# Kernel tuning notes

Measured on AMD Instinct MI355X. Metric: run time of the kernel, lower is better.

## Reference

```python
import jax, jax.numpy as jnp
import numpy as np
from jax import lax

H, W = 3072, 4096
BLACK = 0.0625            # black level (normalized)
KNEE_X = np.array([0.0, 0.25, 1.0], np.float32)   # decompanding curve
KNEE_Y = np.array([0.0, 0.50, 1.0], np.float32)
DEN_R, DEN_EPS = 2, 100.0         # BayerDenoise defaults
AWB_MAX_GAIN = 4.0
LTM_A, LTM_B, LTM_R, LTM_EPS = 0.7, 0.0, 8, 1e-3
GAMMA = 2.2


def _box_sum_1d(x, r, axis):
    """Sliding-window sum of width 2r+1 along `axis`, edge-truncated."""
    n = x.shape[axis]
    c = jnp.cumsum(x, axis=axis)
    hi = jnp.clip(jnp.arange(n) + r, 0, n - 1)
    lo = jnp.arange(n) - r - 1
    upper = jnp.take(c, hi, axis=axis)
    lower = jnp.take(c, jnp.clip(lo, 0, n - 1), axis=axis)
    shp = [1] * x.ndim
    shp[axis] = n
    lower = lower * (lo >= 0).astype(x.dtype).reshape(shp)
    return upper - lower


def box_mean(x, r):
    """2D box mean over last two axes, normalized by valid window counts."""
    s = _box_sum_1d(_box_sum_1d(x, r, -2), r, -1)
    cnt = _box_sum_1d(_box_sum_1d(jnp.ones_like(x), r, -2), r, -1)
    return s / cnt


def guided_self(I, r, eps):
    """Self-guided (edge-preserving) filter."""
    m = box_mean(I, r)
    var = box_mean(I * I, r) - m * m
    a = var / (var + eps)
    b = m * (1.0 - a)
    return box_mean(a, r) * I + box_mean(b, r)


def conv3x3(img, k):
    return lax.conv_general_dilated(img[None, None], k[None, None], (1, 1), 'SAME')[0, 0]


def isp_pipeline(x, ccm):
    # --- DecompandBlackLevel: piecewise-linear decompand + black level ---
    x = jnp.interp(x, jnp.asarray(KNEE_X), jnp.asarray(KNEE_Y))
    x = jnp.clip((x - BLACK) / (1.0 - BLACK), 0.0, 1.0)

    # --- BayerDenoise: guided filter on each RGGB plane ---
    p = jnp.stack([x[0::2, 0::2], x[0::2, 1::2], x[1::2, 0::2], x[1::2, 1::2]])  # [4,H/2,W/2]
    p = guided_self(p, DEN_R, DEN_EPS)

    # --- AWB: gray-world gains from plane means (lum mask [0,1] = all pixels) ---
    r_m, g_m, b_m = p[0].mean(), 0.5 * (p[1].mean() + p[2].mean()), p[3].mean()
    gr = jnp.minimum(g_m / (r_m + 1e-8), AWB_MAX_GAIN)
    gb = jnp.minimum(g_m / (b_m + 1e-8), AWB_MAX_GAIN)
    x = (jnp.zeros_like(x)
         .at[0::2, 0::2].set(jnp.clip(p[0] * gr, 0.0, 1.0))
         .at[0::2, 1::2].set(jnp.clip(p[1], 0.0, 1.0))
         .at[1::2, 0::2].set(jnp.clip(p[2], 0.0, 1.0))
         .at[1::2, 1::2].set(jnp.clip(p[3] * gb, 0.0, 1.0)))

    # --- Demosaic: bilinear on RGGB mosaic ---
    ii = (jnp.arange(H) % 2)[:, None]
    jj = (jnp.arange(W) % 2)[None, :]
    mR = ((ii == 0) & (jj == 0)).astype(x.dtype)
    mG = (ii != jj).astype(x.dtype)
    mB = ((ii == 1) & (jj == 1)).astype(x.dtype)
    k_g = jnp.array([[0, 1, 0], [1, 4, 1], [0, 1, 0]], jnp.float32) / 4.0
    k_rb = jnp.array([[1, 2, 1], [2, 4, 2], [1, 2, 1]], jnp.float32) / 4.0
    rgb = jnp.stack([conv3x3(x * mR, k_rb), conv3x3(x * mG, k_g), conv3x3(x * mB, k_rb)])  # [3,H,W]

    # --- CCM ---
    rgb = jnp.clip(jnp.einsum('ij,jhw->ihw', ccm, rgb), 0.0, 1.0)

    wl = jnp.array([0.299, 0.587, 0.114], jnp.float32)
    Y = jnp.einsum('c,chw->hw', wl, rgb)
    Ys = Y.reshape(H // 2, 2, W // 2, 2).mean(axis=(1, 3))
    base = jax.image.resize(guided_self(Ys, LTM_R, LTM_EPS), (H, W), 'bilinear')
    Ynew = LTM_A * base + LTM_B + (Y - base)       # detail_gain=1, threshold=0
    rgb = jnp.clip(rgb * (Ynew / (Y + 1e-6)), 0.0, 1.0)

    # --- Gamma ---
    rgb = jnp.clip(rgb, 1e-6, 1.0) ** (1.0 / GAMMA)
    # hist_norm / post_denoise / saturation / sharpening are identity at defaults

    # --- RGBtoYUV -> NV12 (full range BT.601) ---
    R, G, B = rgb[0], rgb[1], rgb[2]
    Yf = 0.299 * R + 0.587 * G + 0.114 * B
    U = -0.168736 * R - 0.331264 * G + 0.5 * B + 0.5
    V = 0.5 * R - 0.418688 * G - 0.081312 * B + 0.5
    Us = U.reshape(H // 2, 2, W // 2, 2).mean(axis=(1, 3))
    Vs = V.reshape(H // 2, 2, W // 2, 2).mean(axis=(1, 3))
    uv = jnp.stack([Us, Vs], axis=-1).reshape(H // 2, W)  # interleaved UVUV...
    out = jnp.concatenate([Yf.reshape(-1), uv.reshape(-1)]) * 255.0
    return jnp.clip(out, 0.0, 255.0)   # float NV12 codes (pre-quantization)


def setup_inputs() -> dict:
    key = jax.random.key(0)
    k1, k2 = jax.random.split(key)
    x = jax.random.uniform(k1, (H, W), dtype=jnp.float32)
    ccm = jnp.eye(3, dtype=jnp.float32) + 0.1 * jax.random.normal(k2, (3, 3), dtype=jnp.float32)
    return {"x": x, "ccm": ccm}


def reference(x, ccm):
    return isp_pipeline(x, ccm)
```

## Files before the change

kernel.cpp:

```cpp
#include <hip/hip_runtime.h>
#include <math.h>

#define IMG_H 3072
#define IMG_W 4096
#define Hh 1536
#define Wh 2048
#define S (Hh*Wh)

#define TID 32
#define TIL 16

#if __has_builtin(__builtin_amdgcn_rcpf)
#define RCP(x) __builtin_amdgcn_rcpf(x)
#else
#define RCP(x) (1.0f/(x))
#endif

__device__ __forceinline__ float clamp01(float v){ return fminf(fmaxf(v, 0.0f), 1.0f); }

__device__ __forceinline__ float decompand_black(float v){
  float y = (v <= 0.25f) ? (2.0f*v) : fmaf(v - 0.25f, 0.5f/0.75f, 0.5f);
  y = clamp01(y);
  return clamp01((y - 0.0625f) * (1.0f/0.9375f));
}

__device__ __forceinline__ float gamma22(float x){
  return __builtin_amdgcn_exp2f(0.45454545454545453f * __builtin_amdgcn_logf(x));
}

__global__ __launch_bounds__(256) void k_split(const float* __restrict__ x, float* __restrict__ P,
                                               float* __restrict__ sums){
  int idx = blockIdx.x*256 + threadIdx.x;
  int i = idx >> 10, jq = (idx & 1023)*2;
  const float* r0 = x + (size_t)(2*i)*IMG_W + 2*jq;
  float4 a = *(const float4*)r0;
  float4 b = *(const float4*)(r0 + IMG_W);
  size_t o = (size_t)i*Wh + jq;
  *(float2*)(P + o)            = make_float2(decompand_black(a.x), decompand_black(a.z));
  *(float2*)(P + S + o)        = make_float2(decompand_black(a.y), decompand_black(a.w));
  *(float2*)(P + 2*(size_t)S + o) = make_float2(decompand_black(b.x), decompand_black(b.z));
  *(float2*)(P + 3*(size_t)S + o) = make_float2(decompand_black(b.y), decompand_black(b.w));
  if (blockIdx.x == 0 && threadIdx.x < 4) sums[threadIdx.x] = 0.f;
}

template<int TI, bool FAST>
__device__ __forceinline__ void denoise_col2(const float* __restrict__ in, float* __restrict__ D,
                                             int c0, int i0, float& local){
  const float inv25 = 1.0f/25.0f;
  float cw_a[6], amask[6], cw_o0 = 25.f, cw_o1 = 25.f;
  if (!FAST){
    #pragma unroll
    for (int k=0;k<6;++k){
      int pc = c0 + k - 2;
      bool ok = ((unsigned)pc < (unsigned)Wh);
      amask[k] = ok ? 1.f : 0.f;
      cw_a[k]  = ok ? (float)(min(pc+2, Wh-1) - max(pc-2, 0) + 1) : 1.f;
    }
    cw_o0 = (float)(min(c0+2, Wh-1)   - max(c0-2, 0) + 1);
    cw_o1 = (float)(min(c0+3, Wh-1)   - max(c0-1, 0) + 1);
  }

  float rh1[6][5]={{0}}, rh2[6][5]={{0}};
  float vs1[6]={0}, vs2[6]={0};
  float rha0[5]={0}, rhb0[5]={0}, rha1[5]={0}, rhb1[5]={0};
  float cI0[5]={0}, cI1[5]={0};
  float wa0=0.f, wb0=0.f, wa1=0.f, wb1=0.f;

  const float* rp = in + (size_t)(i0-4)*Wh + c0;
  float* wp = D + (size_t)i0*Wh + c0;

  #pragma unroll 4
  for (int rr=0; rr<TI+8; ++rr){
    int r = i0 - 4 + rr;
    float v[10];
    if (FAST){
      float2 p0 = *(const float2*)(rp-4);
      float2 p1 = *(const float2*)(rp-2);
      float2 p2 = *(const float2*)(rp);
      float2 p3 = *(const float2*)(rp+2);
      float2 p4 = *(const float2*)(rp+4);
      v[0]=p0.x; v[1]=p0.y; v[2]=p1.x; v[3]=p1.y; v[4]=p2.x;
      v[5]=p2.y; v[6]=p3.x; v[7]=p3.y; v[8]=p4.x; v[9]=p4.y;
    } else {
      if ((unsigned)r < (unsigned)Hh){
        #pragma unroll
        for (int d=0; d<10; ++d){
          int c = c0 + d - 4;
          v[d] = ((unsigned)c < (unsigned)Wh) ? rp[d-4] : 0.f;
        }
      } else {
        #pragma unroll
        for (int d=0; d<10; ++d) v[d]=0.f;
      }
    }
    rp += Wh;
    float sq[10];
    #pragma unroll
    for (int d=0; d<10; ++d) sq[d]=v[d]*v[d];
    float h1[6], h2[6];
    h1[0]=v[0]+v[1]+v[2]+v[3]+v[4];
    h2[0]=sq[0]+sq[1]+sq[2]+sq[3]+sq[4];
    #pragma unroll
    for (int k=1;k<6;++k){
      h1[k]=h1[k-1]-v[k-1]+v[k+4];
      h2[k]=h2[k-1]-sq[k-1]+sq[k+4];
    }
    #pragma unroll
    for (int k=0;k<6;++k){
      vs1[k]+=h1[k]-rh1[k][0];
      vs2[k]+=h2[k]-rh2[k][0];
      #pragma unroll
      for (int t=0;t<4;++t){ rh1[k][t]=rh1[k][t+1]; rh2[k][t]=rh2[k][t+1]; }
      rh1[k][4]=h1[k]; rh2[k][4]=h2[k];
    }
    #pragma unroll
    for (int t=0;t<4;++t){ cI0[t]=cI0[t+1]; cI1[t]=cI1[t+1]; }
    cI0[4]=v[4]; cI1[4]=v[5];

    if (rr >= 4){
      int q = r-2;
      float a6[6], b6[6];
      if (FAST){
        #pragma unroll
        for (int k=0;k<6;++k){
          float m   = vs1[k]*inv25;
          float var = fmaf(-m, m, vs2[k]*inv25);
          float a   = var*RCP(var + 100.0f);
          a6[k] = a; b6[k] = fmaf(-m, a, m);
        }
      } else {
        float rmask = ((unsigned)q < (unsigned)Hh) ? 1.f : 0.f;
        float rh = (float)(min(q+2, Hh-1) - max(q-2, 0) + 1);
        #pragma unroll
        for (int k=0;k<6;++k){
          float inv = RCP(rh*cw_a[k]);
          float m   = vs1[k]*inv;
          float var = fmaf(-m, m, vs2[k]*inv);
          float a   = var*RCP(var + 100.0f);
          float b   = fmaf(-m, a, m);
          a6[k] = a*amask[k]*rmask; b6[k] = b*amask[k]*rmask;
        }
      }
      float ha0 = a6[0]+a6[1]+a6[2]+a6[3]+a6[4];
      float hb0 = b6[0]+b6[1]+b6[2]+b6[3]+b6[4];
      float ha1 = ha0 - a6[0] + a6[5];
      float hb1 = hb0 - b6[0] + b6[5];
      wa0 += ha0 - rha0[0]; wb0 += hb0 - rhb0[0];
      wa1 += ha1 - rha1[0]; wb1 += hb1 - rhb1[0];
      #pragma unroll
      for (int t=0;t<4;++t){
        rha0[t]=rha0[t+1]; rhb0[t]=rhb0[t+1];
        rha1[t]=rha1[t+1]; rhb1[t]=rhb1[t+1];
      }
      rha0[4]=ha0; rhb0[4]=hb0; rha1[4]=ha1; rhb1[4]=hb1;

      if (rr >= 8){
        int ro = r-4;
        float invo0, invo1;
        if (FAST){ invo0 = inv25; invo1 = inv25; }
        else {
          float rho = (float)(min(ro+2, Hh-1) - max(ro-2, 0) + 1);
          invo0 = RCP(rho*cw_o0); invo1 = RCP(rho*cw_o1);
        }
        float d0 = fmaf(wa0*invo0, cI0[0], wb0*invo0);
        float d1 = fmaf(wa1*invo1, cI1[0], wb1*invo1);
        *(float2*)wp = make_float2(d0, d1); wp += Wh;
        local += d0 + d1;
      }
    }
  }
}

template<int TI>
__global__ __launch_bounds__(256) void k_denoise(const float* __restrict__ P4,
                                                 float* __restrict__ D4,
                                                 float* __restrict__ sums){
  const int c0 = (blockIdx.x*256 + threadIdx.x)*2;
  const int i0 = blockIdx.y*TI;
  const int pl = blockIdx.z;
  const float* __restrict__ in = P4 + (size_t)pl*S;
  float* __restrict__ D = D4 + (size_t)pl*S;
  float local = 0.f;

  const int cmin = (blockIdx.x*256 + (threadIdx.x & ~63))*2;
  const bool rows_ok = (i0 >= 4) && (i0 + TI + 4 <= Hh);
  const bool fast = rows_ok && (cmin >= 4) && (cmin + 131 < Wh);
  if (fast) denoise_col2<TI, true >(in, D, c0, i0, local);
  else      denoise_col2<TI, false>(in, D, c0, i0, local);

  __shared__ float red[256];
  red[threadIdx.x]=local;
  __syncthreads();
  #pragma unroll
  for (int off=128; off>0; off>>=1){
    if (threadIdx.x<off) red[threadIdx.x]+=red[threadIdx.x+off];
    __syncthreads();
  }
  if (threadIdx.x==0) atomicAdd(sums+pl, red[0]);
}

template<int R, int TI>
__global__ __launch_bounds__(256) void k_boxsq_ab(const float* __restrict__ in,
                                                  float* __restrict__ A, float* __restrict__ B,
                                                  float eps){
  int j  = blockIdx.x*256 + threadIdx.x;
  int i0 = blockIdx.y*TI;
  int cw = min(j+R, Wh-1) - max(j-R, 0) + 1;

  float hs[2*R+1], hs2[2*R+1];
  float ws = 0.f, ws2 = 0.f;
  #pragma unroll
  for (int k=0; k<2*R+1; ++k){
    int r = i0 - R + k;
    float s = 0.f, s2 = 0.f;
    if ((unsigned)r < (unsigned)Hh){
      const float* row = in + r*Wh;
      #pragma unroll
      for (int d=-R; d<=R; ++d){
        int c = j + d;
        float v = ((unsigned)c < (unsigned)Wh) ? row[c] : 0.f;
        s += v; s2 = fmaf(v, v, s2);
      }
    }
    hs[k] = s; hs2[k] = s2; ws += s; ws2 += s2;
  }
  #pragma unroll
  for (int t=0; t<TI; ++t){
    int i = i0 + t;
    int rh = min(i+R, Hh-1) - max(i-R, 0) + 1;
    float inv = 1.0f/(float)(rh*cw);
    float m   = ws*inv;
    float var = fmaf(-m, m, ws2*inv);
    float a   = var/(var + eps);
    A[i*Wh + j] = a;
    B[i*Wh + j] = m*(1.0f - a);
    if (t < TI-1){
      ws -= hs[0]; ws2 -= hs2[0];
      #pragma unroll
      for (int k=0; k<2*R; ++k){ hs[k]=hs[k+1]; hs2[k]=hs2[k+1]; }
      int r = i + R + 1;
      float s = 0.f, s2 = 0.f;
      if (r < Hh){
        const float* row = in + r*Wh;
        #pragma unroll
        for (int d=-R; d<=R; ++d){
          int c = j + d;
          float v = ((unsigned)c < (unsigned)Wh) ? row[c] : 0.f;
          s += v; s2 = fmaf(v, v, s2);
        }
      }
      hs[2*R] = s; hs2[2*R] = s2; ws += s; ws2 += s2;
    }
  }
}

template<int R, int TI>
__global__ __launch_bounds__(256) void k_box_apply(const float* __restrict__ in,
                                                   const float* __restrict__ A, const float* __restrict__ B,
                                                   float* __restrict__ D){
  int j  = blockIdx.x*256 + threadIdx.x;
  int i0 = blockIdx.y*TI;
  int cw = min(j+R, Wh-1) - max(j-R, 0) + 1;

  float ha[2*R+1], hb[2*R+1];
  float wa = 0.f, wb = 0.f;
  #pragma unroll
  for (int k=0; k<2*R+1; ++k){
    int r = i0 - R + k;
    float sa = 0.f, sb = 0.f;
    if ((unsigned)r < (unsigned)Hh){
      const float* ra = A + r*Wh;
      const float* rb = B + r*Wh;
      #pragma unroll
      for (int d=-R; d<=R; ++d){
        int c = j + d;
        bool ok = ((unsigned)c < (unsigned)Wh);
        sa += ok ? ra[c] : 0.f;
        sb += ok ? rb[c] : 0.f;
      }
    }
    ha[k] = sa; hb[k] = sb; wa += sa; wb += sb;
  }
  #pragma unroll
  for (int t=0; t<TI; ++t){
    int i = i0 + t;
    int rh = min(i+R, Hh-1) - max(i-R, 0) + 1;
    float inv = 1.0f/(float)(rh*cw);
    D[i*Wh + j] = fmaf(wa*inv, in[i*Wh + j], wb*inv);
    if (t < TI-1){
      wa -= ha[0]; wb -= hb[0];
      #pragma unroll
      for (int k=0; k<2*R; ++k){ ha[k]=ha[k+1]; hb[k]=hb[k+1]; }
      int r = i + R + 1;
      float sa = 0.f, sb = 0.f;
      if (r < Hh){
        const float* ra = A + r*Wh;
        const float* rb = B + r*Wh;
        #pragma unroll
        for (int d2=-R; d2<=R; ++d2){
          int c = j + d2;
          bool ok = ((unsigned)c < (unsigned)Wh);
          sa += ok ? ra[c] : 0.f;
          sb += ok ? rb[c] : 0.f;
        }
      }
      ha[2*R] = sa; hb[2*R] = sb; wa += sa; wb += sb;
    }
  }
}

__device__ __forceinline__ void awb_gains(const float* __restrict__ sums, float& gr, float& gb){
  const float invS = 1.0f/(float)S;
  float rm = sums[0]*invS, g1 = sums[1]*invS, g2 = sums[2]*invS, bm = sums[3]*invS;
  float gm = 0.5f*(g1+g2);
  gr = fminf(gm/(rm + 1e-8f), 4.0f);
  gb = fminf(gm/(bm + 1e-8f), 4.0f);
}

__device__ __forceinline__ void load_mosaic2(const float* __restrict__ D, float gr, float gb,
                                             int i, int j, float m[4][6]){
  const float* __restrict__ P0 = D;
  const float* __restrict__ P1 = D + (size_t)S;
  const float* __restrict__ P2 = D + (size_t)2*S;
  const float* __restrict__ P3 = D + (size_t)3*S;
  const bool up = (i > 0), dn = (i < Hh-1), lf = (j > 0), rt = (j+2 < Wh);
  const size_t rc = (size_t)i*Wh + j;
  const size_t ru = rc - Wh, rd = rc + Wh;
  const float2 z = make_float2(0.f, 0.f);
  {
    float2 t3 = up ? *(const float2*)(P3+ru) : z;
    float2 t2 = up ? *(const float2*)(P2+ru) : z;
    m[0][0] = (up&&lf) ? clamp01(P3[ru-1]*gb) : 0.f;
    m[0][1] = clamp01(t2.x);
    m[0][2] = clamp01(t3.x*gb);
    m[0][3] = clamp01(t2.y);
    m[0][4] = clamp01(t3.y*gb);
    m[0][5] = (up&&rt) ? clamp01(P2[ru+2]) : 0.f;
  }
  {
    float2 t1 = *(const float2*)(P1+rc);
    float2 t0 = *(const float2*)(P0+rc);
    m[1][0] = lf ? clamp01(P1[rc-1]) : 0.f;
    m[1][1] = clamp01(t0.x*gr);
    m[1][2] = clamp01(t1.x);
    m[1][3] = clamp01(t0.y*gr);
    m[1][4] = clamp01(t1.y);
    m[1][5] = rt ? clamp01(P0[rc+2]*gr) : 0.f;
  }
  {
    float2 s3 = *(const float2*)(P3+rc);
    float2 s2 = *(const float2*)(P2+rc);
    m[2][0] = lf ? clamp01(P3[rc-1]*gb) : 0.f;
    m[2][1] = clamp01(s2.x);
    m[2][2] = clamp01(s3.x*gb);
    m[2][3] = clamp01(s2.y);
    m[2][4] = clamp01(s3.y*gb);
    m[2][5] = rt ? clamp01(P2[rc+2]) : 0.f;
  }
  {
    float2 u1 = dn ? *(const float2*)(P1+rd) : z;
    float2 u0 = dn ? *(const float2*)(P0+rd) : z;
    m[3][0] = (dn&&lf) ? clamp01(P1[rd-1]) : 0.f;
    m[3][1] = clamp01(u0.x*gr);
    m[3][2] = clamp01(u1.x);
    m[3][3] = clamp01(u0.y*gr);
    m[3][4] = clamp01(u1.y);
    m[3][5] = (dn&&rt) ? clamp01(P0[rd+2]*gr) : 0.f;
  }
}

template<int O>
__device__ __forceinline__ void demosaic_ccm_s(const float m[4][6], const float* __restrict__ C,
                                               float R[2][2], float G[2][2], float Bv[2][2]){
  #define MM(a,b) m[a][(b)+2*O]
  float r[2][2], g[2][2], b[2][2];
  r[0][0] = MM(1,1);
  g[0][0] = 0.25f*(MM(0,1)+MM(2,1)+MM(1,0)+MM(1,2));
  b[0][0] = 0.25f*(MM(0,0)+MM(0,2)+MM(2,0)+MM(2,2));
  r[0][1] = 0.5f*(MM(1,1)+MM(1,3));
  g[0][1] = MM(1,2);
  b[0][1] = 0.5f*(MM(0,2)+MM(2,2));
  r[1][0] = 0.5f*(MM(1,1)+MM(3,1));
  g[1][0] = MM(2,1);
  b[1][0] = 0.5f*(MM(2,0)+MM(2,2));
  r[1][1] = 0.25f*(MM(1,1)+MM(1,3)+MM(3,1)+MM(3,3));
  g[1][1] = 0.25f*(MM(1,2)+MM(3,2)+MM(2,1)+MM(2,3));
  b[1][1] = MM(2,2);
  #undef MM
  #pragma unroll
  for (int a=0; a<2; ++a){
    #pragma unroll
    for (int c=0; c<2; ++c){
      R[a][c]  = clamp01(fmaf(C[2], b[a][c], fmaf(C[1], g[a][c], C[0]*r[a][c])));
      G[a][c]  = clamp01(fmaf(C[5], b[a][c], fmaf(C[4], g[a][c], C[3]*r[a][c])));
      Bv[a][c] = clamp01(fmaf(C[8], b[a][c], fmaf(C[7], g[a][c], C[6]*r[a][c])));
    }
  }
}

__global__ __launch_bounds__(256) void k_ys(const float* __restrict__ D, const float* __restrict__ sums,
                                            const float* __restrict__ C, float* __restrict__ Ys){
  int idx = blockIdx.x*256 + threadIdx.x;
  int i = idx >> 10, j = (idx & 1023)*2;
  float gr, gb; awb_gains(sums, gr, gb);
  float m[4][6]; load_mosaic2(D, gr, gb, i, j, m);
  float y0 = 0.f, y1 = 0.f;
  {
    float R[2][2], G[2][2], Bv[2][2];
    demosaic_ccm_s<0>(m, C, R, G, Bv);
    #pragma unroll
    for (int a=0; a<2; ++a)
      #pragma unroll
      for (int c=0; c<2; ++c)
        y0 += 0.299f*R[a][c] + 0.587f*G[a][c] + 0.114f*Bv[a][c];
  }
  {
    float R[2][2], G[2][2], Bv[2][2];
    demosaic_ccm_s<1>(m, C, R, G, Bv);
    #pragma unroll
    for (int a=0; a<2; ++a)
      #pragma unroll
      for (int c=0; c<2; ++c)
        y1 += 0.299f*R[a][c] + 0.587f*G[a][c] + 0.114f*Bv[a][c];
  }
  *(float2*)(Ys + (size_t)i*Wh + j) = make_float2(0.25f*y0, 0.25f*y1);
}

__global__ __launch_bounds__(256) void k_final(const float* __restrict__ D, const float* __restrict__ sums,
                                               const float* __restrict__ C,
                                               const float* __restrict__ bs, float* __restrict__ out){
  int idx = blockIdx.x*256 + threadIdx.x;
  int i = idx >> 10, j = (idx & 1023)*2;
  float gr, gb; awb_gains(sums, gr, gb);
  float m[4][6]; load_mosaic2(D, gr, gb, i, j, m);

  float bsv[3][4];
  #pragma unroll
  for (int a=0; a<3; ++a){
    int r = min(max(i-1+a, 0), Hh-1);
    const float* br = bs + ((size_t)r<<11);
    bsv[a][0] = br[max(j-1, 0)];
    float2 t = *(const float2*)(br + j);
    bsv[a][1] = t.x; bsv[a][2] = t.y;
    bsv[a][3] = br[min(j+2, Wh-1)];
  }

  float Yrow0[4], Yrow1[4], UV[4];
  #pragma unroll
  for (int o=0; o<2; ++o){
    float R[2][2], G[2][2], Bv[2][2];
    if (o==0) demosaic_ccm_s<0>(m, C, R, G, Bv);
    else      demosaic_ccm_s<1>(m, C, R, G, Bv);
    float base[2][2];
    base[0][0] = 0.0625f*bsv[0][0+o] + 0.1875f*bsv[0][1+o] + 0.1875f*bsv[1][0+o] + 0.5625f*bsv[1][1+o];
    base[0][1] = 0.1875f*bsv[0][1+o] + 0.0625f*bsv[0][2+o] + 0.5625f*bsv[1][1+o] + 0.1875f*bsv[1][2+o];
    base[1][0] = 0.1875f*bsv[1][0+o] + 0.5625f*bsv[1][1+o] + 0.0625f*bsv[2][0+o] + 0.1875f*bsv[2][1+o];
    base[1][1] = 0.5625f*bsv[1][1+o] + 0.1875f*bsv[1][2+o] + 0.1875f*bsv[2][1+o] + 0.0625f*bsv[2][2+o];

    float Uacc = 0.f, Vacc = 0.f;
    #pragma unroll
    for (int a=0; a<2; ++a){
      #pragma unroll
      for (int c=0; c<2; ++c){
        float Yl   = 0.299f*R[a][c] + 0.587f*G[a][c] + 0.114f*Bv[a][c];
        float Ynew = fmaf(0.7f, base[a][c], Yl - base[a][c]);
        float sc   = Ynew/(Yl + 1e-6f);
        float Rg = gamma22(fmaxf(clamp01(R[a][c]*sc),  1e-6f));
        float Gg = gamma22(fmaxf(clamp01(G[a][c]*sc),  1e-6f));
        float Bg = gamma22(fmaxf(clamp01(Bv[a][c]*sc), 1e-6f));
        float Yf = 0.299f*Rg + 0.587f*Gg + 0.114f*Bg;
        float Yq = fminf(fmaxf(Yf*255.0f, 0.0f), 255.0f);
        if (a==0) Yrow0[2*o+c] = Yq; else Yrow1[2*o+c] = Yq;
        Uacc += -0.168736f*Rg - 0.331264f*Gg + 0.5f*Bg + 0.5f;
        Vacc +=  0.5f*Rg - 0.418688f*Gg - 0.081312f*Bg + 0.5f;
      }
    }
    UV[2*o]   = fminf(fmaxf(0.25f*Uacc*255.0f, 0.0f), 255.0f);
    UV[2*o+1] = fminf(fmaxf(0.25f*Vacc*255.0f, 0.0f), 255.0f);
  }
  *(float4*)(out + (size_t)(2*i)*IMG_W   + 2*j) = make_float4(Yrow0[0], Yrow0[1], Yrow0[2], Yrow0[3]);
  *(float4*)(out + (size_t)(2*i+1)*IMG_W + 2*j) = make_float4(Yrow1[0], Yrow1[1], Yrow1[2], Yrow1[3]);
  *(float4*)(out + (size_t)IMG_H*IMG_W + (size_t)i*IMG_W + 2*j) = make_float4(UV[0], UV[1], UV[2], UV[3]);
}

extern "C" void kernel_launch(void* const* d_in, const int* in_sizes, int n_in,
                              void* d_out, int out_size, void* d_ws, size_t ws_size,
                              hipStream_t stream){
  const float* x   = (const float*)d_in[0];
  const float* ccm = (const float*)d_in[1];
  float* ws  = (float*)d_ws;
  float* out = (float*)d_out;

  size_t need = ((size_t)10*S + 8)*sizeof(float);
  if (ws_size < need) return;

  float* P  = ws;
  float* D  = ws + (size_t)4*S;
  float* Ys = ws + (size_t)8*S;
  float* La = ws + (size_t)9*S;
  float* Lb = ws;
  float* bs = ws + (size_t)S;
  float* sums  = ws + (size_t)10*S;

  const int nb2 = S/512;
  dim3 gdn(Wh/512, Hh/TID, 4);
  dim3 gltm(Wh/256, Hh/TIL);

  k_split<<<nb2, 256, 0, stream>>>(x, P, sums);
  k_denoise<TID><<<gdn, 256, 0, stream>>>(P, D, sums);
  k_ys<<<nb2, 256, 0, stream>>>(D, sums, ccm, Ys);
  k_boxsq_ab<8, TIL><<<gltm, 256, 0, stream>>>(Ys, La, Lb, 1e-3f);
  k_box_apply<8, TIL><<<gltm, 256, 0, stream>>>(Ys, La, Lb, bs);
  k_final<<<nb2, 256, 0, stream>>>(D, sums, ccm, bs, out);
}
```

Before: 322.0 us.

## Split LTM box filters into separable horizontal scan and vertical sliding passes

Replaces the two fused 2D box-filter kernels with four separable passes. Horizontal passes use a wave-level prefix scan via shuffles to form 17-wide row sums. Vertical passes use running sums down each column to form the guided-filter coefficients and the final output. This removes the 17 redundant horizontal loads per row in the old kernels, at the cost of two extra launches and extra global round-trips through intermediate buffers.

```diff
diff --git a/kernel.cpp b/kernel.cpp
--- a/kernel.cpp
+++ b/kernel.cpp
@@ -8,7 +8,8 @@
 #define S (Hh*Wh)
 
 #define TID 32
-#define TIL 16
+#define TVL 16
+#define HBLK 192
 
 #if __has_builtin(__builtin_amdgcn_rcpf)
 #define RCP(x) __builtin_amdgcn_rcpf(x)
@@ -199,112 +200,107 @@
   if (threadIdx.x==0) atomicAdd(sums+pl, red[0]);
 }
 
-template<int R, int TI>
-__global__ __launch_bounds__(256) void k_boxsq_ab(const float* __restrict__ in,
-                                                  float* __restrict__ A, float* __restrict__ B,
-                                                  float eps){
-  int j  = blockIdx.x*256 + threadIdx.x;
-  int i0 = blockIdx.y*TI;
-  int cw = min(j+R, Wh-1) - max(j-R, 0) + 1;
-
-  float hs[2*R+1], hs2[2*R+1];
-  float ws = 0.f, ws2 = 0.f;
-  #pragma unroll
-  for (int k=0; k<2*R+1; ++k){
-    int r = i0 - R + k;
-    float s = 0.f, s2 = 0.f;
+template<bool SQUARE>
+__global__ __launch_bounds__(256) void k_ltm_h(const float* __restrict__ X1,
+                                               const float* __restrict__ X2,
+                                               float* __restrict__ O1,
+                                               float* __restrict__ O2){
+  const int lane = threadIdx.x & 63;
+  const int wave = threadIdx.x >> 6;
+  const int row  = blockIdx.y;
+  const int ob   = blockIdx.x*HBLK + wave*48;
+  const int c    = ob - 8 + lane;
+  const size_t rb = (size_t)row*Wh;
+
+  float v1 = 0.f, v2 = 0.f;
+  if ((unsigned)c < (unsigned)Wh){
+    v1 = X1[rb + c];
+    v2 = SQUARE ? v1*v1 : X2[rb + c];
+  }
+  #pragma unroll
+  for (int d=1; d<64; d<<=1){
+    float t1 = __shfl_up(v1, d, 64);
+    float t2 = __shfl_up(v2, d, 64);
+    if (lane >= d){ v1 += t1; v2 += t2; }
+  }
+  float hi1 = __shfl_down(v1, 16, 64);
+  float hi2 = __shfl_down(v2, 16, 64);
+  float lo1 = __shfl_up(v1, 1, 64);
+  float lo2 = __shfl_up(v2, 1, 64);
+  if (lane == 0){ lo1 = 0.f; lo2 = 0.f; }
+  int oc = ob + lane;
+  if (lane < 48 && oc < Wh){
+    O1[rb + oc] = hi1 - lo1;
+    O2[rb + oc] = hi2 - lo2;
+  }
+}
+
+template<int TV>
+__global__ __launch_bounds__(256) void k_ltm_v_ab(const float* __restrict__ H1,
+                                                  const float* __restrict__ H2,
+                                                  float* __restrict__ A,
+                                                  float* __restrict__ B){
+  const int j  = blockIdx.x*256 + threadIdx.x;
+  const int i0 = blockIdx.y*TV;
+  const float cwf = (float)(min(j+8, Wh-1) - max(j-8, 0) + 1);
+  float ws1 = 0.f, ws2 = 0.f;
+  #pragma unroll
+  for (int k=-8; k<=8; ++k){
+    int r = i0 + k;
     if ((unsigned)r < (unsigned)Hh){
-      const float* row = in + r*Wh;
-      #pragma unroll
-      for (int d=-R; d<=R; ++d){
-        int c = j + d;
-        float v = ((unsigned)c < (unsigned)Wh) ? row[c] : 0.f;
-        s += v; s2 = fmaf(v, v, s2);
-      }
-    }
-    hs[k] = s; hs2[k] = s2; ws += s; ws2 += s2;
-  }
-  #pragma unroll
-  for (int t=0; t<TI; ++t){
+      ws1 += H1[(size_t)r*Wh + j];
+      ws2 += H2[(size_t)r*Wh + j];
+    }
+  }
+  #pragma unroll
+  for (int t=0; t<TV; ++t){
     int i = i0 + t;
-    int rh = min(i+R, Hh-1) - max(i-R, 0) + 1;
-    float inv = 1.0f/(float)(rh*cw);
-    float m   = ws*inv;
+    float rhf = (float)(min(i+8, Hh-1) - max(i-8, 0) + 1);
+    float inv = 1.0f/(rhf*cwf);
+    float m   = ws1*inv;
     float var = fmaf(-m, m, ws2*inv);
-    float a   = var/(var + eps);
-    A[i*Wh + j] = a;
-    B[i*Wh + j] = m*(1.0f - a);
-    if (t < TI-1){
-      ws -= hs[0]; ws2 -= hs2[0];
-      #pragma unroll
-      for (int k=0; k<2*R; ++k){ hs[k]=hs[k+1]; hs2[k]=hs2[k+1]; }
-      int r = i + R + 1;
-      float s = 0.f, s2 = 0.f;
-      if (r < Hh){
-        const float* row = in + r*Wh;
-        #pragma unroll
-        for (int d=-R; d<=R; ++d){
-          int c = j + d;
-          float v = ((unsigned)c < (unsigned)Wh) ? row[c] : 0.f;
-          s += v; s2 = fmaf(v, v, s2);
-        }
-      }
-      hs[2*R] = s; hs2[2*R] = s2; ws += s; ws2 += s2;
-    }
-  }
-}
-
-template<int R, int TI>
-__global__ __launch_bounds__(256) void k_box_apply(const float* __restrict__ in,
-                                                   const float* __restrict__ A, const float* __restrict__ B,
-                                                   float* __restrict__ D){
-  int j  = blockIdx.x*256 + threadIdx.x;
-  int i0 = blockIdx.y*TI;
-  int cw = min(j+R, Wh-1) - max(j-R, 0) + 1;
-
-  float ha[2*R+1], hb[2*R+1];
+    float a   = var/(var + 1e-3f);
+    A[(size_t)i*Wh + j] = a;
+    B[(size_t)i*Wh + j] = m*(1.0f - a);
+    if (t < TV-1){
+      int rn = i+9, ro = i-8;
+      float n1=0.f, n2=0.f, o1=0.f, o2=0.f;
+      if (rn < Hh){ n1 = H1[(size_t)rn*Wh + j]; n2 = H2[(size_t)rn*Wh + j]; }
+      if (ro >= 0){ o1 = H1[(size_t)ro*Wh + j]; o2 = H2[(size_t)ro*Wh + j]; }
+      ws1 += n1 - o1; ws2 += n2 - o2;
+    }
+  }
+}
+
+template<int TV>
+__global__ __launch_bounds__(256) void k_ltm_v_fin(const float* __restrict__ Ha,
+                                                   const float* __restrict__ Hb,
+                                                   const float* __restrict__ Ysrc,
+                                                   float* __restrict__ bs){
+  const int j  = blockIdx.x*256 + threadIdx.x;
+  const int i0 = blockIdx.y*TV;
+  const float cwf = (float)(min(j+8, Wh-1) - max(j-8, 0) + 1);
   float wa = 0.f, wb = 0.f;
   #pragma unroll
-  for (int k=0; k<2*R+1; ++k){
-    int r = i0 - R + k;
-    float sa = 0.f, sb = 0.f;
+  for (int k=-8; k<=8; ++k){
+    int r = i0 + k;
     if ((unsigned)r < (unsigned)Hh){
-      const float* ra = A + r*Wh;
-      const float* rb = B + r*Wh;
-      #pragma unroll
-      for (int d=-R; d<=R; ++d){
-        int c = j + d;
-        bool ok = ((unsigned)c < (unsigned)Wh);
-        sa += ok ? ra[c] : 0.f;
-        sb += ok ? rb[c] : 0.f;
-      }
-    }
-    ha[k] = sa; hb[k] = sb; wa += sa; wb += sb;
-  }
-  #pragma unroll
-  for (int t=0; t<TI; ++t){
+      wa += Ha[(size_t)r*Wh + j];
+      wb += Hb[(size_t)r*Wh + j];
+    }
+  }
+  #pragma unroll
+  for (int t=0; t<TV; ++t){
     int i = i0 + t;
-    int rh = min(i+R, Hh-1) - max(i-R, 0) + 1;
-    float inv = 1.0f/(float)(rh*cw);
-    D[i*Wh + j] = fmaf(wa*inv, in[i*Wh + j], wb*inv);
-    if (t < TI-1){
-      wa -= ha[0]; wb -= hb[0];
-      #pragma unroll
-      for (int k=0; k<2*R; ++k){ ha[k]=ha[k+1]; hb[k]=hb[k+1]; }
-      int r = i + R + 1;
-      float sa = 0.f, sb = 0.f;
-      if (r < Hh){
-        const float* ra = A + r*Wh;
-        const float* rb = B + r*Wh;
-        #pragma unroll
-        for (int d2=-R; d2<=R; ++d2){
-          int c = j + d2;
-          bool ok = ((unsigned)c < (unsigned)Wh);
-          sa += ok ? ra[c] : 0.f;
-          sb += ok ? rb[c] : 0.f;
-        }
-      }
-      ha[2*R] = sa; hb[2*R] = sb; wa += sa; wb += sb;
+    float rhf = (float)(min(i+8, Hh-1) - max(i-8, 0) + 1);
+    float inv = 1.0f/(rhf*cwf);
+    bs[(size_t)i*Wh + j] = fmaf(wa*inv, Ysrc[(size_t)i*Wh + j], wb*inv);
+    if (t < TV-1){
+      int rn = i+9, ro = i-8;
+      float na=0.f, nb=0.f, oa=0.f, ob_=0.f;
+      if (rn < Hh){ na = Ha[(size_t)rn*Wh + j]; nb = Hb[(size_t)rn*Wh + j]; }
+      if (ro >= 0){ oa = Ha[(size_t)ro*Wh + j]; ob_ = Hb[(size_t)ro*Wh + j]; }
+      wa += na - oa; wb += nb - ob_;
     }
   }
 }
@@ -494,22 +490,29 @@
   size_t need = ((size_t)10*S + 8)*sizeof(float);
   if (ws_size < need) return;
 
-  float* P  = ws;
-  float* D  = ws + (size_t)4*S;
-  float* Ys = ws + (size_t)8*S;
-  float* La = ws + (size_t)9*S;
-  float* Lb = ws;
-  float* bs = ws + (size_t)S;
-  float* sums  = ws + (size_t)10*S;
+  float* P   = ws;
+  float* D   = ws + (size_t)4*S;
+  float* Ys  = ws + (size_t)8*S;
+  float* Hs1 = ws;
+  float* Hs2 = ws + (size_t)S;
+  float* A   = ws + (size_t)2*S;
+  float* Bb  = ws + (size_t)3*S;
+  float* Ha  = ws;
+  float* Hb  = ws + (size_t)S;
+  float* bs  = ws + (size_t)2*S;
+  float* sums = ws + (size_t)10*S;
 
   const int nb2 = S/512;
   dim3 gdn(Wh/512, Hh/TID, 4);
-  dim3 gltm(Wh/256, Hh/TIL);
+  dim3 gh((Wh + HBLK - 1)/HBLK, Hh);
+  dim3 gv(Wh/256, Hh/TVL);
 
   k_split<<<nb2, 256, 0, stream>>>(x, P, sums);
   k_denoise<TID><<<gdn, 256, 0, stream>>>(P, D, sums);
   k_ys<<<nb2, 256, 0, stream>>>(D, sums, ccm, Ys);
-  k_boxsq_ab<8, TIL><<<gltm, 256, 0, stream>>>(Ys, La, Lb, 1e-3f);
-  k_box_apply<8, TIL><<<gltm, 256, 0, stream>>>(Ys, La, Lb, bs);
+  k_ltm_h<true ><<<gh, 256, 0, stream>>>(Ys, Ys, Hs1, Hs2);
+  k_ltm_v_ab<TVL><<<gv, 256, 0, stream>>>(Hs1, Hs2, A, Bb);
+  k_ltm_h<false><<<gh, 256, 0, stream>>>(A, Bb, Ha, Hb);
+  k_ltm_v_fin<TVL><<<gv, 256, 0, stream>>>(Ha, Hb, Ys, bs);
   k_final<<<nb2, 256, 0, stream>>>(D, sums, ccm, bs, out);
 }
```

Result: faster. 285.9 us (-11.2%).
